# Performance work log

Hardware: AMD Instinct MI355X
Metric: run time of the kernel (lower is better)

## Reference

```python
import jax, jax.numpy as jnp
import numpy as np

B, L, D = 4096, 200, 32
NUM_USERS, NUM_GOODS, NUM_CATS = 49023, 143534, 4815
ATT_H1, ATT_H2 = 80, 40
MLP_H1, MLP_H2 = 200, 80
NEG_INF = jnp.float32(-2**32 + 1)


def prelu(x, a):
    return jnp.where(x >= 0, x, a * x)


def setup_inputs() -> dict:
    key = jax.random.key(0)
    ks = jax.random.split(key, 24)
    g = lambda k, shape, fan_in: jax.random.normal(k, shape, jnp.float32) * (1.0 / np.sqrt(fan_in))
    return {
        "uid": jax.random.randint(ks[0], (B,), 0, NUM_USERS, jnp.int32),
        "gid": jax.random.randint(ks[1], (B,), 0, NUM_GOODS, jnp.int32),
        "cid": jax.random.randint(ks[2], (B,), 0, NUM_CATS, jnp.int32),
        "gid_his": jax.random.randint(ks[3], (B, L), 0, NUM_GOODS, jnp.int32),
        "cid_his": jax.random.randint(ks[4], (B, L), 0, NUM_CATS, jnp.int32),
        "masks": jax.random.randint(ks[5], (B, L), 0, 2, jnp.int32),
        # frozen embedding tables
        "user_emb": jax.random.normal(ks[6], (NUM_USERS, D), jnp.float32),
        "good_emb": jax.random.normal(ks[7], (NUM_GOODS, D), jnp.float32),
        "cat_emb": jax.random.normal(ks[8], (NUM_CATS, D), jnp.float32),
        # attention MLP: 8D -> 80 -> 40 -> 1, sigmoid activations
        "att_w1": g(ks[9], (ATT_H1, 8 * D), 8 * D), "att_b1": jnp.zeros((ATT_H1,), jnp.float32),
        "att_w2": g(ks[10], (ATT_H2, ATT_H1), ATT_H1), "att_b2": jnp.zeros((ATT_H2,), jnp.float32),
        "att_w3": g(ks[11], (1, ATT_H2), ATT_H2), "att_b3": jnp.zeros((1,), jnp.float32),
        # final MLP: 9D -> 200 -> 80 -> 2, PReLU activations
        "mlp_w1": g(ks[12], (MLP_H1, 9 * D), 9 * D), "mlp_b1": jnp.zeros((MLP_H1,), jnp.float32),
        "mlp_w2": g(ks[13], (MLP_H2, MLP_H1), MLP_H1), "mlp_b2": jnp.zeros((MLP_H2,), jnp.float32),
        "mlp_w3": g(ks[14], (2, MLP_H2), MLP_H2), "mlp_b3": jnp.zeros((2,), jnp.float32),
        "a1": jnp.full((MLP_H1,), 0.25, jnp.float32),
        "a2": jnp.full((MLP_H2,), 0.25, jnp.float32),
    }


def reference(uid, gid, cid, gid_his, cid_his, masks,
              user_emb, good_emb, cat_emb,
              att_w1, att_b1, att_w2, att_b2, att_w3, att_b3,
              mlp_w1, mlp_b1, mlp_w2, mlp_b2, mlp_w3, mlp_b3, a1, a2):
    user = user_emb[uid]                                              # (B, D)
    query = jnp.concatenate([good_emb[gid], cat_emb[cid]], -1)        # (B, 2D)
    beh = jnp.concatenate([good_emb[gid_his], cat_emb[cid_his]], -1)  # (B, L, 2D)

    # attention: concat(query, behavior, diff, product) -> tiny MLP -> masked softmax pool
    q = jnp.broadcast_to(query[:, None, :], beh.shape)                # (B, L, 2D)
    s = jnp.concatenate([q, beh, q - beh, q * beh], -1)               # (B, L, 8D)
    s = jax.nn.sigmoid(jnp.einsum('blk,hk->blh', s, att_w1) + att_b1)
    s = jax.nn.sigmoid(jnp.einsum('blh,gh->blg', s, att_w2) + att_b2)
    s = jnp.einsum('blg,og->blo', s, att_w3) + att_b3                 # (B, L, 1)
    s = jnp.where(masks[..., None].astype(bool), s, NEG_INF)
    w = jax.nn.softmax(s, axis=1)
    att = jnp.sum(w * beh, axis=1)                                    # (B, 2D)

    ubs = beh.sum(axis=1)                                             # (B, 2D)
    x = jnp.concatenate([user, query, ubs, ubs * query, att], -1)     # (B, 9D)
    x = prelu(x @ mlp_w1.T + mlp_b1, a1)
    x = prelu(x @ mlp_w2.T + mlp_b2, a2)
    return x @ mlp_w3.T + mlp_b3                                      # (B, 2)
```

## Files before the change

### kernel.cpp

```cpp
#include <hip/hip_runtime.h>
#include <math.h>

typedef unsigned short u16;
typedef unsigned int u32;
typedef __attribute__((ext_vector_type(8))) short short8;
typedef __attribute__((ext_vector_type(8))) float f32x8;
typedef __attribute__((ext_vector_type(4))) float f32x4;
typedef __attribute__((ext_vector_type(2))) unsigned int uint2v;

#define NEG_BIG   (-4294967296.0f)
#define NEG_INF_F (-__builtin_inff())

#define WS_S    0
#define WS_W1T  5120
#define WS_W2T  62720
#define WS_W3T  78720
#define WS_W3P  78880
#define WS_WF1F 78928
#define WS_WF2F 84048
#define WS_XF   86352

__device__ __forceinline__ u32 f2bf2(float lo, float hi) {
    u32 r;
    asm("v_cvt_pk_bf16_f32 %0, %1, %2" : "=v"(r) : "v"(lo), "v"(hi));
    return r;
}
__device__ __forceinline__ u16 f2bf(float f) {
    u32 r;
    asm("v_cvt_pk_bf16_f32 %0, %1, %1" : "=v"(r) : "v"(f));
    return (u16)r;
}
__device__ __forceinline__ float bf2f(u16 h) {
    union { u32 u; float f; } v; v.u = ((u32)h) << 16;
    return v.f;
}
__device__ __forceinline__ float fsigmoid(float x) {
    float e, r;
    float t = x * -1.44269504088896f;
    asm("v_exp_f32 %0, %1" : "=v"(e) : "v"(t));
    float d = 1.0f + e;
    asm("v_rcp_f32 %0, %1" : "=v"(r) : "v"(d));
    return r;
}
__device__ __forceinline__ short8 mulqf(short8 a, f32x8 qf) {
    union { u32 w[4]; short8 s; } r;
    #pragma unroll
    for (int j = 0; j < 4; ++j) {
        float p0 = bf2f((u16)a[2*j])   * qf[2*j];
        float p1 = bf2f((u16)a[2*j+1]) * qf[2*j+1];
        r.w[j] = f2bf2(p0, p1);
    }
    return r.s;
}
__device__ __forceinline__ f32x4 mfma16(short8 a, short8 b, f32x4 c) {
    return __builtin_amdgcn_mfma_f32_16x16x32_bf16(a, b, c, 0, 0, 0);
}

__global__ __launch_bounds__(256) void prep_kernel(
    const float* __restrict__ att_w1,
    const float* __restrict__ att_w2,
    const float* __restrict__ att_w3,
    const float* __restrict__ mlp_w1,
    const float* __restrict__ mlp_w2,
    const float* __restrict__ mlp_w3,
    float* __restrict__ ws)
{
    int idx = blockIdx.x * 256 + threadIdx.x;
    if (idx < 5120) {
        int h = idx >> 6, j = idx & 63;
        ws[WS_S + idx] = att_w1[h*256 + j] + att_w1[h*256 + 128 + j];
    } else if (idx < 62720) {
        int r = idx - 5120;
        int k = r / 200, t = r - k*200;
        ws[WS_W1T + r] = mlp_w1[t*288 + k];
    } else if (idx < 78720) {
        int r = idx - 62720;
        int k = r / 80, g = r - k*80;
        ws[WS_W2T + r] = mlp_w2[g*200 + k];
    } else if (idx < 78880) {
        int r = idx - 78720;
        int k = r >> 1, o = r & 1;
        ws[WS_W3T + r] = mlp_w3[o*80 + k];
    } else if (idx < 78928) {
        int g = idx - 78880;
        ws[WS_W3P + g] = (g < 40) ? att_w3[g] : 0.0f;
    } else if (idx < 89168) {
        int e  = idx - 78928;
        int nt = e >> 11;
        int ks = (e >> 9) & 3;
        int ln = (e >> 3) & 63;
        int j  = e & 7;
        int n = nt*16 + (ln & 15);
        int k = ks*32 + (ln >> 4)*8 + j;
        float val = (k < 64)
            ? (att_w1[n*256 + 64 + k] - att_w1[n*256 + 128 + k])
            : att_w1[n*256 + 192 + (k - 64)];
        ((u16*)(ws + WS_WF1F))[e] = f2bf(val);
    } else if (idx < 93776) {
        int e  = idx - 89168;
        int nt = e / 1536;
        int ks = (e / 512) % 3;
        int ln = (e >> 3) & 63;
        int j  = e & 7;
        int n = nt*16 + (ln & 15);
        int k = ks*32 + (ln >> 4)*8 + j;
        float val = (n < 40 && k < 80) ? att_w2[n*80 + k] : 0.0f;
        ((u16*)(ws + WS_WF2F))[e] = f2bf(val);
    }
}

__global__ __launch_bounds__(256, 2) void din_kernel(
    const int* __restrict__ uid, const int* __restrict__ gid, const int* __restrict__ cid,
    const int* __restrict__ gid_his, const int* __restrict__ cid_his, const int* __restrict__ masks,
    const float* __restrict__ user_emb, const float* __restrict__ good_emb, const float* __restrict__ cat_emb,
    const float* __restrict__ att_b1, const float* __restrict__ att_b2, const float* __restrict__ att_b3,
    const float* __restrict__ ws, float* __restrict__ Xg)
{
    __shared__ u16 Xc[200*64];
    __shared__ u16 scr[4*1664];
    __shared__ float q_sh[64];
    __shared__ float c0_sh[80];
    __shared__ float sp_sh[256];
    __shared__ float scal_sh[2];

    float* redA  = (float*)scr;
    float* redU  = redA + 512;

    const int b    = blockIdx.x;
    const int tid  = threadIdx.x;
    const int lane = tid & 63;
    const int wv   = tid >> 6;
    const int lrow = lane & 15;
    const int lgrp = lane >> 4;

    const int* gh = gid_his + b*200;
    const int* ch = cid_his + b*200;

    short8 wf1r[20];
    short8 wf2r[9];
    float  w3v[10];
    {
        const short8* WF1 = (const short8*)(ws + WS_WF1F);
        const short8* WF2 = (const short8*)(ws + WS_WF2F);
        #pragma unroll
        for (int i = 0; i < 20; ++i) wf1r[i] = WF1[i*64 + lane];
        #pragma unroll
        for (int i = 0; i < 9; ++i)  wf2r[i] = WF2[i*64 + lane];
        #pragma unroll
        for (int i = 0; i < 10; ++i) w3v[i] = ws[WS_W3P + lgrp + 4*i];
    }

    #pragma unroll
    for (int it = 0; it < 12; ++it) {
        int idx = it*256 + tid;
        int l = idx >> 4, c = idx & 15;
        const float* src = (c < 8)
            ? (good_emb + (size_t)gh[l]*32 + (c & 7)*4)
            : (cat_emb  + (size_t)ch[l]*32 + (c & 7)*4);
        float4 v = *(const float4*)src;
        uint2v pk;
        pk[0] = f2bf2(v.x, v.y);
        pk[1] = f2bf2(v.z, v.w);
        int byteoff = l*128 + ((((c >> 1) ^ (l & 7)) << 4)) + ((c & 1) << 3);
        *((uint2v*)((char*)Xc + byteoff)) = pk;
    }
    if (tid < 128) {
        int idx = 3072 + tid;
        int l = idx >> 4, c = idx & 15;
        const float* src = (c < 8)
            ? (good_emb + (size_t)gh[l]*32 + (c & 7)*4)
            : (cat_emb  + (size_t)ch[l]*32 + (c & 7)*4);
        float4 v = *(const float4*)src;
        uint2v pk;
        pk[0] = f2bf2(v.x, v.y);
        pk[1] = f2bf2(v.z, v.w);
        int byteoff = l*128 + ((((c >> 1) ^ (l & 7)) << 4)) + ((c & 1) << 3);
        *((uint2v*)((char*)Xc + byteoff)) = pk;
    }
    if (tid < 64) {
        q_sh[tid] = (tid < 32) ? good_emb[(size_t)gid[b]*32 + tid]
                               : cat_emb[(size_t)cid[b]*32 + (tid - 32)];
    }
    if (tid >= 200 && tid < 256) sp_sh[tid] = NEG_INF_F;
    __syncthreads();

    if (tid < 80) {
        const float4* Sw = (const float4*)(ws + WS_S + tid*64);
        const float4* q4 = (const float4*)q_sh;
        float u0 = 0.f, u1 = 0.f;
        #pragma unroll
        for (int j = 0; j < 16; j += 2) {
            float4 w0 = Sw[j],   qv0 = q4[j];
            float4 w1 = Sw[j+1], qv1 = q4[j+1];
            u0 += w0.x*qv0.x + w0.y*qv0.y + w0.z*qv0.z + w0.w*qv0.w;
            u1 += w1.x*qv1.x + w1.y*qv1.y + w1.z*qv1.z + w1.w*qv1.w;
        }
        c0_sh[tid] = att_b1[tid] + u0 + u1;
    }
    __syncthreads();

    f32x8 qf0, qf1;
    #pragma unroll
    for (int j = 0; j < 8; ++j) {
        qf0[j] = q_sh[lgrp*8 + j];
        qf1[j] = q_sh[32 + lgrp*8 + j];
    }
    float c0v[5];
    #pragma unroll
    for (int nt = 0; nt < 5; ++nt) c0v[nt] = c0_sh[nt*16 + lrow];
    float b2v[3];
    #pragma unroll
    for (int nt = 0; nt < 3; ++nt) {
        int col = nt*16 + lrow;
        b2v[nt] = (col < 40) ? att_b2[col] : 0.0f;
    }
    const float bias3 = att_b3[0];

    u16*   scr_w = scr + wv*1664;
    float* scr_f = (float*)scr_w;

    {
        uint2v z; z[0] = 0u; z[1] = 0u;
        *((uint2v*)(scr_w + lrow*104 + 80 + lgrp*4)) = z;
    }

    for (int t = wv; t < 13; t += 4) {
        const int m0 = (t == 12) ? 184 : (t << 4);
        const int m  = m0 + lrow;

        short8 A0, A1;
        {
            int sl0 = (0 + lgrp) ^ (m & 7);
            int sl1 = (4 + lgrp) ^ (m & 7);
            A0 = *(const short8*)((const char*)Xc + m*128 + (sl0 << 4));
            A1 = *(const short8*)((const char*)Xc + m*128 + (sl1 << 4));
        }
        short8 A2 = mulqf(A0, qf0);
        short8 A3 = mulqf(A1, qf1);

        #pragma unroll
        for (int nt = 0; nt < 5; ++nt) {
            f32x4 acc = {0.f, 0.f, 0.f, 0.f};
            acc = mfma16(A0, wf1r[nt*4 + 0], acc);
            acc = mfma16(A1, wf1r[nt*4 + 1], acc);
            acc = mfma16(A2, wf1r[nt*4 + 2], acc);
            acc = mfma16(A3, wf1r[nt*4 + 3], acc);
            #pragma unroll
            for (int r = 0; r < 4; ++r) {
                float s1v = fsigmoid(acc[r] + c0v[nt]);
                scr_w[(lgrp*4 + r)*104 + nt*16 + lrow] = f2bf(s1v);
            }
        }

        short8 B0 = *(const short8*)(scr_w + lrow*104 +  0 + lgrp*8);
        short8 B1 = *(const short8*)(scr_w + lrow*104 + 32 + lgrp*8);
        short8 B2 = *(const short8*)(scr_w + lrow*104 + 64 + lgrp*8);
        #pragma unroll
        for (int nt = 0; nt < 3; ++nt) {
            f32x4 acc = {0.f, 0.f, 0.f, 0.f};
            acc = mfma16(B0, wf2r[nt*3 + 0], acc);
            acc = mfma16(B1, wf2r[nt*3 + 1], acc);
            acc = mfma16(B2, wf2r[nt*3 + 2], acc);
            #pragma unroll
            for (int r = 0; r < 4; ++r) {
                float s2v = fsigmoid(acc[r] + b2v[nt]);
                scr_f[(lgrp*4 + r)*52 + nt*16 + lrow] = s2v;
            }
        }

        float v3 = 0.f;
        #pragma unroll
        for (int i = 0; i < 10; ++i) {
            v3 += scr_f[lrow*52 + lgrp + 4*i] * w3v[i];
        }
        v3 += __shfl_xor(v3, 16);
        v3 += __shfl_xor(v3, 32);
        if (lane < 16) {
            int mm = m0 + lane;
            float sval = v3 + bias3;
            int mk = masks[b*200 + mm];
            sp_sh[mm] = mk ? sval : NEG_BIG;
        }
    }
    __syncthreads();

    if (tid < 64) {
        float mv = fmaxf(fmaxf(sp_sh[tid], sp_sh[tid+64]), fmaxf(sp_sh[tid+128], sp_sh[tid+192]));
        #pragma unroll
        for (int off = 32; off > 0; off >>= 1) mv = fmaxf(mv, __shfl_down(mv, off));
        if (tid == 0) scal_sh[0] = mv;
    }
    __syncthreads();
    {
        float mx = scal_sh[0];
        float sm = sp_sh[tid];
        float ev = (tid < 200) ? __expf(sm - mx) : 0.0f;
        sp_sh[tid] = ev;
    }
    __syncthreads();
    if (tid < 64) {
        float s = (sp_sh[tid] + sp_sh[tid+64]) + (sp_sh[tid+128] + sp_sh[tid+192]);
        #pragma unroll
        for (int off = 32; off > 0; off >>= 1) s += __shfl_down(s, off);
        if (tid == 0) scal_sh[1] = s;
    }
    __syncthreads();

    {
        int j2 = tid & 31;
        int qq = tid >> 5;
        int slot = j2 >> 2;
        int inb  = (j2 & 3) << 2;
        float a0 = 0.f, a1 = 0.f, u0 = 0.f, u1 = 0.f;
        #pragma unroll 5
        for (int mm = qq*25; mm < qq*25 + 25; ++mm) {
            u32 pr = *(const u32*)((const char*)Xc + mm*128 + (((slot ^ (mm & 7)) << 4)) + inb);
            float b0 = bf2f((u16)pr);
            float b1_ = bf2f((u16)(pr >> 16));
            float w = sp_sh[mm];
            a0 += w*b0; a1 += w*b1_;
            u0 += b0;   u1 += b1_;
        }
        redA[qq*64 + 2*j2]     = a0;
        redA[qq*64 + 2*j2 + 1] = a1;
        redU[qq*64 + 2*j2]     = u0;
        redU[qq*64 + 2*j2 + 1] = u1;
    }
    __syncthreads();

    float inv = 1.0f / scal_sh[1];
    if (tid < 64) {
        float att = 0.f, ub = 0.f;
        #pragma unroll
        for (int qq = 0; qq < 8; ++qq) {
            att += redA[qq*64 + tid];
            ub  += redU[qq*64 + tid];
        }
        att *= inv;
        float qv = q_sh[tid];
        float* xr = Xg + (size_t)b*288;
        xr[32  + tid] = qv;
        xr[96  + tid] = ub;
        xr[160 + tid] = ub * qv;
        xr[224 + tid] = att;
    }
    if (tid >= 64 && tid < 96) {
        Xg[(size_t)b*288 + (tid - 64)] = user_emb[(size_t)uid[b]*32 + (tid - 64)];
    }
}

__global__ __launch_bounds__(256) void mlp_kernel(
    const float* __restrict__ ws,
    const float* __restrict__ mlp_b1, const float* __restrict__ mlp_b2, const float* __restrict__ mlp_b3,
    const float* __restrict__ pa1, const float* __restrict__ pa2,
    float* __restrict__ out)
{
    __shared__ float h1_sh[8*204];
    __shared__ float h2_sh[8*81];

    const int tid = threadIdx.x;
    const int r0  = blockIdx.x * 8;
    const float* Xg  = ws + WS_XF;
    const float* w1T = ws + WS_W1T;
    const float* w2T = ws + WS_W2T;
    const float* w3T = ws + WS_W3T;

    {
        int n = (tid < 200) ? tid : 199;
        float bias = mlp_b1[n];
        float acc[8];
        #pragma unroll
        for (int r = 0; r < 8; ++r) acc[r] = bias;
        for (int k = 0; k < 288; k += 4) {
            float w0 = w1T[(k+0)*200 + n];
            float w1 = w1T[(k+1)*200 + n];
            float w2 = w1T[(k+2)*200 + n];
            float w3 = w1T[(k+3)*200 + n];
            #pragma unroll
            for (int r = 0; r < 8; ++r) {
                const float4 xv = *(const float4*)(Xg + (size_t)(r0 + r)*288 + k);
                acc[r] += xv.x*w0 + xv.y*w1 + xv.z*w2 + xv.w*w3;
            }
        }
        if (tid < 200) {
            float a = pa1[n];
            #pragma unroll
            for (int r = 0; r < 8; ++r) {
                float v = acc[r];
                h1_sh[r*204 + n] = (v >= 0.f) ? v : a*v;
            }
        }
    }
    __syncthreads();

    if (tid < 160) {
        int g  = (tid < 80) ? tid : tid - 80;
        int rh = (tid < 80) ? 0 : 4;
        float bias = mlp_b2[g];
        float acc[4];
        #pragma unroll
        for (int r = 0; r < 4; ++r) acc[r] = bias;
        for (int k = 0; k < 200; k += 4) {
            float w0 = w2T[(k+0)*80 + g];
            float w1 = w2T[(k+1)*80 + g];
            float w2 = w2T[(k+2)*80 + g];
            float w3 = w2T[(k+3)*80 + g];
            #pragma unroll
            for (int r = 0; r < 4; ++r) {
                const float4 xv = *(const float4*)(&h1_sh[(rh + r)*204 + k]);
                acc[r] += xv.x*w0 + xv.y*w1 + xv.z*w2 + xv.w*w3;
            }
        }
        float a = pa2[g];
        #pragma unroll
        for (int r = 0; r < 4; ++r) {
            float v = acc[r];
            h2_sh[(rh + r)*81 + g] = (v >= 0.f) ? v : a*v;
        }
    }
    __syncthreads();

    if (tid < 16) {
        int r = tid >> 1, o = tid & 1;
        float acc = mlp_b3[o];
        #pragma unroll 8
        for (int k = 0; k < 80; ++k) acc += h2_sh[r*81 + k] * w3T[k*2 + o];
        out[(size_t)(r0 + r)*2 + o] = acc;
    }
}

extern "C" void kernel_launch(void* const* d_in, const int* in_sizes, int n_in,
                              void* d_out, int out_size, void* d_ws, size_t ws_size,
                              hipStream_t stream) {
    const int*   uid      = (const int*)d_in[0];
    const int*   gid      = (const int*)d_in[1];
    const int*   cid      = (const int*)d_in[2];
    const int*   gid_his  = (const int*)d_in[3];
    const int*   cid_his  = (const int*)d_in[4];
    const int*   masks    = (const int*)d_in[5];
    const float* user_emb = (const float*)d_in[6];
    const float* good_emb = (const float*)d_in[7];
    const float* cat_emb  = (const float*)d_in[8];
    const float* att_w1   = (const float*)d_in[9];
    const float* att_b1   = (const float*)d_in[10];
    const float* att_w2   = (const float*)d_in[11];
    const float* att_b2   = (const float*)d_in[12];
    const float* att_w3   = (const float*)d_in[13];
    const float* att_b3   = (const float*)d_in[14];
    const float* mlp_w1   = (const float*)d_in[15];
    const float* mlp_b1   = (const float*)d_in[16];
    const float* mlp_w2   = (const float*)d_in[17];
    const float* mlp_b2   = (const float*)d_in[18];
    const float* mlp_w3   = (const float*)d_in[19];
    const float* mlp_b3   = (const float*)d_in[20];
    const float* pa1      = (const float*)d_in[21];
    const float* pa2      = (const float*)d_in[22];
    float* ws   = (float*)d_ws;
    float* outp = (float*)d_out;

    hipLaunchKernelGGL(prep_kernel, dim3(367), dim3(256), 0, stream,
                       att_w1, att_w2, att_w3, mlp_w1, mlp_w2, mlp_w3, ws);
    hipLaunchKernelGGL(din_kernel, dim3(4096), dim3(256), 0, stream,
                       uid, gid, cid, gid_his, cid_his, masks,
                       user_emb, good_emb, cat_emb,
                       att_b1, att_b2, att_b3,
                       ws, ws + WS_XF);
    hipLaunchKernelGGL(mlp_kernel, dim3(512), dim3(256), 0, stream,
                       ws, mlp_b1, mlp_b2, mlp_b3, pa1, pa2, outp);
}
```

Baseline: 149.4 us.

## Stage history indices in LDS, fuse behavior sum into gather, interleave pooling rows

History indices are first copied into shared memory, so each thread gathers a fixed column of embedding rows. The unweighted behavior sum is now taken in fp32 during the gather instead of from the bf16 copy in the pooling pass, which removes half the pooling reads and accumulators. The attention pooling loop now interleaves rows by phase (row = 8*i + phase) with a fixed swizzle, so its addresses are simpler. This adds an extra barrier and a 16-way partial-sum reduction through scratch shared memory.

```diff
diff --git a/kernel.cpp b/kernel.cpp
--- a/kernel.cpp
+++ b/kernel.cpp
@@ -121,10 +121,10 @@
     __shared__ float q_sh[64];
     __shared__ float c0_sh[80];
     __shared__ float sp_sh[256];
+    __shared__ float ub_sh[64];
     __shared__ float scal_sh[2];
 
-    float* redA  = (float*)scr;
-    float* redU  = redA + 512;
+    float* redA = (float*)scr;
 
     const int b    = blockIdx.x;
     const int tid  = threadIdx.x;
@@ -150,39 +150,50 @@
         for (int i = 0; i < 10; ++i) w3v[i] = ws[WS_W3P + lgrp + 4*i];
     }
 
-    #pragma unroll
-    for (int it = 0; it < 12; ++it) {
-        int idx = it*256 + tid;
-        int l = idx >> 4, c = idx & 15;
-        const float* src = (c < 8)
-            ? (good_emb + (size_t)gh[l]*32 + (c & 7)*4)
-            : (cat_emb  + (size_t)ch[l]*32 + (c & 7)*4);
-        float4 v = *(const float4*)src;
-        uint2v pk;
-        pk[0] = f2bf2(v.x, v.y);
-        pk[1] = f2bf2(v.z, v.w);
-        int byteoff = l*128 + ((((c >> 1) ^ (l & 7)) << 4)) + ((c & 1) << 3);
-        *((uint2v*)((char*)Xc + byteoff)) = pk;
-    }
-    if (tid < 128) {
-        int idx = 3072 + tid;
-        int l = idx >> 4, c = idx & 15;
-        const float* src = (c < 8)
-            ? (good_emb + (size_t)gh[l]*32 + (c & 7)*4)
-            : (cat_emb  + (size_t)ch[l]*32 + (c & 7)*4);
-        float4 v = *(const float4*)src;
-        uint2v pk;
-        pk[0] = f2bf2(v.x, v.y);
-        pk[1] = f2bf2(v.z, v.w);
-        int byteoff = l*128 + ((((c >> 1) ^ (l & 7)) << 4)) + ((c & 1) << 3);
-        *((uint2v*)((char*)Xc + byteoff)) = pk;
+    int* idxg = (int*)scr;
+    int* idxc = idxg + 200;
+    if (tid < 200) {
+        idxg[tid] = gh[tid];
+        idxc[tid] = ch[tid];
     }
     if (tid < 64) {
         q_sh[tid] = (tid < 32) ? good_emb[(size_t)gid[b]*32 + tid]
                                : cat_emb[(size_t)cid[b]*32 + (tid - 32)];
     }
-    if (tid >= 200 && tid < 256) sp_sh[tid] = NEG_INF_F;
-    __syncthreads();
+    if (tid >= 200) sp_sh[tid] = NEG_INF_F;
+    __syncthreads();
+
+    const int c  = tid & 15;
+    const int lg = tid >> 4;
+    {
+        const float* bptr = ((c < 8) ? good_emb : cat_emb) + ((c & 7) << 2);
+        const int*   idxp = (c < 8) ? idxg : idxc;
+        char* xdst = (char*)Xc + lg*128 + ((((c >> 1) ^ (lg & 7)) << 4)) + ((c & 1) << 3);
+        float4 ub4 = {0.f, 0.f, 0.f, 0.f};
+        #pragma unroll
+        for (int it = 0; it < 12; ++it) {
+            int id = idxp[it*16 + lg];
+            float4 v = *(const float4*)(bptr + (size_t)id*32);
+            ub4.x += v.x; ub4.y += v.y; ub4.z += v.z; ub4.w += v.w;
+            uint2v pk;
+            pk[0] = f2bf2(v.x, v.y);
+            pk[1] = f2bf2(v.z, v.w);
+            *((uint2v*)(xdst + it*2048)) = pk;
+        }
+        if (lg < 8) {
+            int id = idxp[192 + lg];
+            float4 v = *(const float4*)(bptr + (size_t)id*32);
+            ub4.x += v.x; ub4.y += v.y; ub4.z += v.z; ub4.w += v.w;
+            uint2v pk;
+            pk[0] = f2bf2(v.x, v.y);
+            pk[1] = f2bf2(v.z, v.w);
+            *((uint2v*)(xdst + 12*2048)) = pk;
+        }
+        __syncthreads();
+
+        float* pubs = (float*)scr;
+        *((float4*)(pubs + lg*64 + c*4)) = ub4;
+    }
 
     if (tid < 80) {
         const float4* Sw = (const float4*)(ws + WS_S + tid*64);
@@ -196,6 +207,15 @@
             u1 += w1.x*qv1.x + w1.y*qv1.y + w1.z*qv1.z + w1.w*qv1.w;
         }
         c0_sh[tid] = att_b1[tid] + u0 + u1;
+    }
+    __syncthreads();
+
+    if (tid < 64) {
+        const float* pubs = (const float*)scr;
+        float s = 0.f;
+        #pragma unroll
+        for (int g = 0; g < 16; ++g) s += pubs[g*64 + tid];
+        ub_sh[tid] = s;
     }
     __syncthreads();
 
@@ -307,41 +327,36 @@
     __syncthreads();
 
     {
-        int j2 = tid & 31;
-        int qq = tid >> 5;
-        int slot = j2 >> 2;
-        int inb  = (j2 & 3) << 2;
-        float a0 = 0.f, a1 = 0.f, u0 = 0.f, u1 = 0.f;
-        #pragma unroll 5
-        for (int mm = qq*25; mm < qq*25 + 25; ++mm) {
-            u32 pr = *(const u32*)((const char*)Xc + mm*128 + (((slot ^ (mm & 7)) << 4)) + inb);
-            float b0 = bf2f((u16)pr);
-            float b1_ = bf2f((u16)(pr >> 16));
-            float w = sp_sh[mm];
-            a0 += w*b0; a1 += w*b1_;
-            u0 += b0;   u1 += b1_;
-        }
-        redA[qq*64 + 2*j2]     = a0;
-        redA[qq*64 + 2*j2 + 1] = a1;
-        redU[qq*64 + 2*j2]     = u0;
-        redU[qq*64 + 2*j2 + 1] = u1;
+        int j2     = tid & 31;
+        int rphase = tid >> 5;
+        int cbase  = ((((j2 >> 2) ^ rphase)) << 4) + ((j2 & 3) << 2);
+        const char* xrow = (const char*)Xc + rphase*128 + cbase;
+        const float* sprow = sp_sh + rphase;
+        float a0 = 0.f, a1 = 0.f;
+        #pragma unroll
+        for (int i = 0; i < 25; ++i) {
+            u32 pr = *(const u32*)(xrow + i*1024);
+            float w = sprow[i*8];
+            a0 += w * bf2f((u16)pr);
+            a1 += w * bf2f((u16)(pr >> 16));
+        }
+        redA[rphase*64 + 2*j2]     = a0;
+        redA[rphase*64 + 2*j2 + 1] = a1;
     }
     __syncthreads();
 
     float inv = 1.0f / scal_sh[1];
     if (tid < 64) {
-        float att = 0.f, ub = 0.f;
-        #pragma unroll
-        for (int qq = 0; qq < 8; ++qq) {
-            att += redA[qq*64 + tid];
-            ub  += redU[qq*64 + tid];
-        }
+        float att = 0.f;
+        #pragma unroll
+        for (int rp = 0; rp < 8; ++rp) att += redA[rp*64 + tid];
         att *= inv;
-        float qv = q_sh[tid];
+        float ubv = ub_sh[tid];
+        float qv  = q_sh[tid];
         float* xr = Xg + (size_t)b*288;
         xr[32  + tid] = qv;
-        xr[96  + tid] = ub;
-        xr[160 + tid] = ub * qv;
+        xr[96  + tid] = ubv;
+        xr[160 + tid] = ubv * qv;
         xr[224 + tid] = att;
     }
     if (tid >= 64 && tid < 96) {
```

New measurement: 173.7 us. 16.3% more time.
